# Performance work log

Hardware: AMD Instinct MI355X
Metric: run time of the kernel (lower is better)

Reference implementation:

```python
import jax, jax.numpy as jnp
import numpy as np

NEG_SLOPE = 0.01  # F.leaky_relu default in GATLayer.edge_attention
N_NODES = 50000
N_EDGES = 1600000
IN_DIM = 128
HEADS = 8
D_HEAD = 16  # out_dim / head_num = 128 / 8


def setup_inputs() -> dict:
    key = jax.random.key(0)
    ks = jax.random.split(key, 9)
    # glorot-ish scales for linear projections and attention vectors
    w_scale = (2.0 / (IN_DIM + D_HEAD)) ** 0.5
    a_scale = (2.0 / (2 * D_HEAD + 1)) ** 0.5
    return {
        "x": jax.random.normal(ks[0], (N_NODES, IN_DIM), dtype=jnp.float32),
        "src": jax.random.randint(ks[1], (N_EDGES,), 0, N_NODES, dtype=jnp.int32),
        "dst": jax.random.randint(ks[2], (N_EDGES,), 0, N_NODES, dtype=jnp.int32),
        "W1": jax.random.normal(ks[3], (HEADS, IN_DIM, D_HEAD), dtype=jnp.float32) * w_scale,
        "a1_src": jax.random.normal(ks[4], (HEADS, D_HEAD), dtype=jnp.float32) * a_scale,
        "a1_dst": jax.random.normal(ks[5], (HEADS, D_HEAD), dtype=jnp.float32) * a_scale,
        "W2": jax.random.normal(ks[6], (HEADS, IN_DIM, D_HEAD), dtype=jnp.float32) * w_scale,
        "a2_src": jax.random.normal(ks[7], (HEADS, D_HEAD), dtype=jnp.float32) * a_scale,
        "a2_dst": jax.random.normal(ks[8], (HEADS, D_HEAD), dtype=jnp.float32) * a_scale,
    }


def gat_multihead(h, src, dst, W, a_src, a_dst, num_nodes):
    """One MultiHeadLayer(GATLayer) with concat merge. h: [N, Din]."""
    z = jnp.einsum("nd,hdk->nhk", h, W)            # [N,H,Dh] per-head projection
    # attn_fc(cat(z_src, z_dst)) == a_src . z_src + a_dst . z_dst
    s_src = jnp.einsum("nhk,hk->nh", z, a_src)      # [N,H]
    s_dst = jnp.einsum("nhk,hk->nh", z, a_dst)      # [N,H]
    e = jax.nn.leaky_relu(s_src[src] + s_dst[dst], NEG_SLOPE)  # [E,H]
    # segment softmax over incoming edges of each dst node
    e_max = jax.ops.segment_max(e, dst, num_segments=num_nodes)          # [N,H]
    e_max = jnp.where(jnp.isfinite(e_max), e_max, 0.0)                   # empty segments
    w = jnp.exp(e - e_max[dst])                                          # [E,H]
    denom = jax.ops.segment_sum(w, dst, num_segments=num_nodes)          # [N,H]
    msg = w[:, :, None] * z[src]                                         # [E,H,Dh]
    num = jax.ops.segment_sum(msg, dst, num_segments=num_nodes)          # [N,H,Dh]
    out = num / jnp.where(denom == 0.0, 1.0, denom)[:, :, None]
    return out.reshape(num_nodes, -1)                                    # concat heads -> [N, H*Dh]


def reference(x, src, dst, W1, a1_src, a1_dst, W2, a2_src, a2_dst):
    n = x.shape[0]
    h = gat_multihead(x, src, dst, W1, a1_src, a1_dst, n)
    h = jax.nn.elu(h)
    h = gat_multihead(h, src, dst, W2, a2_src, a2_dst, n)
    return h
```

## Files before the change

### kernel.cpp

```cpp
#include <hip/hip_runtime.h>
#include <hip/hip_bf16.h>

#define N_NODES 50000
#define N_EDGES 1600000
#define NEG_SLOPE 0.01f
#define WPAD 136

#define NBKT 256
#define BKTW 196
#define NBLK1 200
#define CHUNK1 8000

typedef _Float16 v8h __attribute__((ext_vector_type(8)));
typedef _Float16 v2h __attribute__((ext_vector_type(2)));
typedef float v4f __attribute__((ext_vector_type(4)));

__global__ __launch_bounds__(256) void proj_mfma_kernel(
    const float* __restrict__ x,
    const float* __restrict__ W,
    _Float16* __restrict__ z)
{
    __shared__ _Float16 Wl[128 * WPAD];
    __shared__ _Float16 Zs[4][16][132];

    const int t = threadIdx.x;
    for (int i = t; i < 16384; i += 256) {
        const int h = i >> 11, k = (i >> 4) & 127, col = i & 15;
        Wl[(h * 16 + col) * WPAD + k] = (_Float16)W[i];
    }
    __syncthreads();

    const int wid = t >> 6;
    const int l   = t & 63;
    const int lc  = l & 15;
    const int kg  = l >> 4;

    const int nwaves = gridDim.x * 4;
    for (int tile = blockIdx.x * 4 + wid; tile < N_NODES / 16; tile += nwaves) {
        const int n0 = tile * 16;
        v4f acc[8];
#pragma unroll
        for (int ht = 0; ht < 8; ht++) acc[ht] = (v4f)0.f;

#pragma unroll
        for (int kb = 0; kb < 4; kb++) {
            const float4* xp = (const float4*)&x[(n0 + lc) * 128 + kb * 32 + kg * 8];
            const float4 xa = xp[0];
            const float4 xb = xp[1];
            v8h a;
            a[0] = (_Float16)xa.x; a[1] = (_Float16)xa.y;
            a[2] = (_Float16)xa.z; a[3] = (_Float16)xa.w;
            a[4] = (_Float16)xb.x; a[5] = (_Float16)xb.y;
            a[6] = (_Float16)xb.z; a[7] = (_Float16)xb.w;
#pragma unroll
            for (int ht = 0; ht < 8; ht++) {
                const v8h b = *(const v8h*)&Wl[(ht * 16 + lc) * WPAD + kb * 32 + kg * 8];
                acc[ht] = __builtin_amdgcn_mfma_f32_16x16x32_f16(a, b, acc[ht], 0, 0, 0);
            }
        }

#pragma unroll
        for (int ht = 0; ht < 8; ht++)
#pragma unroll
            for (int i = 0; i < 4; i++)
                Zs[wid][4 * kg + i][ht * 16 + lc] = (_Float16)acc[ht][i];

        const int r = l >> 2, q = l & 3;
        const _Float16* zr = &Zs[wid][r][q * 32];
        _Float16* zg = &z[(n0 + r) * 128 + q * 32];
#pragma unroll
        for (int c = 0; c < 4; c++)
            *(v8h*)(zg + c * 8) = *(const v8h*)(zr + c * 8);
    }
}

__global__ __launch_bounds__(256) void score_kernel(
    const _Float16* __restrict__ z,
    const float* __restrict__ a_src, const float* __restrict__ a_dst,
    float* __restrict__ s_src, float* __restrict__ s_dst)
{
    __shared__ float asl[128], adl[128];
    const int t = threadIdx.x;
    if (t < 128) { asl[t] = a_src[t]; adl[t] = a_dst[t]; }
    __syncthreads();

    const int idx = blockIdx.x * 256 + t;
    if (idx >= N_NODES * 8) return;
    const int n = idx >> 3, h = idx & 7;

    const v8h z0 = *(const v8h*)&z[n * 128 + h * 16];
    const v8h z1 = *(const v8h*)&z[n * 128 + h * 16 + 8];
    float ss = 0.f, sd = 0.f;
#pragma unroll
    for (int j = 0; j < 8; j++) {
        ss = fmaf((float)z0[j], asl[h * 16 + j], ss);
        sd = fmaf((float)z0[j], adl[h * 16 + j], sd);
    }
#pragma unroll
    for (int j = 0; j < 8; j++) {
        ss = fmaf((float)z1[j], asl[h * 16 + 8 + j], ss);
        sd = fmaf((float)z1[j], adl[h * 16 + 8 + j], sd);
    }
    s_src[idx] = ss;
    s_dst[idx] = sd;
}

__global__ __launch_bounds__(256) void hist_bucket_kernel(
    const int* __restrict__ dst, int* __restrict__ bh)
{
    __shared__ int lhist[NBKT];
    const int t = threadIdx.x, blk = blockIdx.x;
    lhist[t] = 0;
    __syncthreads();
    const int4* d4 = (const int4*)(dst + blk * CHUNK1);
    for (int i = t; i < CHUNK1 / 4; i += 256) {
        const int4 d = d4[i];
        atomicAdd(&lhist[(unsigned)d.x / BKTW], 1);
        atomicAdd(&lhist[(unsigned)d.y / BKTW], 1);
        atomicAdd(&lhist[(unsigned)d.z / BKTW], 1);
        atomicAdd(&lhist[(unsigned)d.w / BKTW], 1);
    }
    __syncthreads();
    bh[t * NBLK1 + blk] = lhist[t];
}

__global__ __launch_bounds__(256) void scan_buckets_kernel(
    int* __restrict__ bh, int* __restrict__ btotal)
{
    __shared__ int sb[256];
    const int t = threadIdx.x, b = blockIdx.x;
    const int v = (t < NBLK1) ? bh[b * NBLK1 + t] : 0;
    sb[t] = v;
    __syncthreads();
    int x = v;
    for (int off = 1; off < 256; off <<= 1) {
        const int add = (t >= off) ? sb[t - off] : 0;
        __syncthreads();
        x += add;
        sb[t] = x;
        __syncthreads();
    }
    if (t < NBLK1) bh[b * NBLK1 + t] = x - v;
    if (t == 255) btotal[b] = x;
}

__global__ __launch_bounds__(256) void scan_totals_kernel(
    const int* __restrict__ btotal, int* __restrict__ bstart)
{
    __shared__ int sb[256];
    const int t = threadIdx.x;
    const int v = btotal[t];
    sb[t] = v;
    __syncthreads();
    int x = v;
    for (int off = 1; off < 256; off <<= 1) {
        const int add = (t >= off) ? sb[t - off] : 0;
        __syncthreads();
        x += add;
        sb[t] = x;
        __syncthreads();
    }
    bstart[t] = x - v;
    if (t == 255) bstart[256] = x;
}

__global__ __launch_bounds__(256) void scatter_bucket_kernel(
    const int* __restrict__ src, const int* __restrict__ dst,
    const int* __restrict__ bh, const int* __restrict__ bstart,
    int* __restrict__ gbuf)
{
    __shared__ int lbase[NBKT];
    __shared__ int lcur[NBKT];
    const int t = threadIdx.x, blk = blockIdx.x;
    lbase[t] = bstart[t] + bh[t * NBLK1 + blk];
    lcur[t] = 0;
    __syncthreads();
    const int4* s4 = (const int4*)(src + blk * CHUNK1);
    const int4* d4 = (const int4*)(dst + blk * CHUNK1);
    for (int i = t; i < CHUNK1 / 4; i += 256) {
        const int4 d = d4[i];
        const int4 s = s4[i];
#pragma unroll
        for (int u = 0; u < 4; u++) {
            const int dd = (u == 0) ? d.x : (u == 1) ? d.y : (u == 2) ? d.z : d.w;
            const int ss = (u == 0) ? s.x : (u == 1) ? s.y : (u == 2) ? s.z : s.w;
            const unsigned b = (unsigned)dd / BKTW;
            const int ld = dd - (int)b * BKTW;
            const int r = atomicAdd(&lcur[b], 1);
            gbuf[lbase[b] + r] = (ld << 16) | ss;
        }
    }
}

__global__ __launch_bounds__(256) void sort_bucket_kernel(
    const int* __restrict__ gbuf, const int* __restrict__ bstart,
    int* __restrict__ perm, int* __restrict__ rowp)
{
    __shared__ int lhist[NBKT];
    __shared__ int lscan[NBKT];
    __shared__ int lcur[NBKT];
    const int t = threadIdx.x, b = blockIdx.x;
    const int base = bstart[b];
    const int cnt  = bstart[b + 1] - base;
    const int n0   = b * BKTW;

    lhist[t] = 0;
    lcur[t] = 0;
    __syncthreads();
    for (int i = t; i < cnt; i += 256)
        atomicAdd(&lhist[gbuf[base + i] >> 16], 1);
    __syncthreads();

    const int v = lhist[t];
    lscan[t] = v;
    __syncthreads();
    int x = v;
    for (int off = 1; off < 256; off <<= 1) {
        const int add = (t >= off) ? lscan[t - off] : 0;
        __syncthreads();
        x += add;
        lscan[t] = x;
        __syncthreads();
    }
    const int excl = x - v;
    __syncthreads();
    lscan[t] = excl;

    const int n = n0 + t;
    if (t < BKTW && n < N_NODES) rowp[n] = base + excl;
    if (b == NBKT - 1 && t == 0) rowp[N_NODES] = bstart[NBKT];
    __syncthreads();

    for (int i = t; i < cnt; i += 256) {
        const int e = gbuf[base + i];
        const int ld = e >> 16;
        const int r = atomicAdd(&lcur[ld], 1);
        perm[base + lscan[ld] + r] = (e & 0xFFFF) << 8;
    }
}

__global__ __launch_bounds__(256) void gather_kernel(
    const int* __restrict__ row_ptr, const int* __restrict__ perm,
    const char* __restrict__ zb,
    const char* __restrict__ ssb,
    const float* __restrict__ s_dst,
    float* __restrict__ out, const int apply_elu)
{
    const int wv = threadIdx.x >> 6;
    const int l  = threadIdx.x & 63;
    const int n  = blockIdx.x * 4 + wv;

    const int e8 = l >> 3;
    const int h8 = l & 7;
    const int h  = l >> 3;

    const int start = row_ptr[n];
    const int end   = row_ptr[n + 1];
    const float sd8 = s_dst[n * 8 + h8];

    float acc0 = 0.f, acc1 = 0.f, wsum = 0.f;

    for (int j0 = start; j0 < end; j0 += 8) {
        const int off = perm[j0 + e8];
        float s = *(const float*)(ssb + (off >> 3) + h8 * 4) + sd8;
        s = s > 0.f ? s : NEG_SLOPE * s;
        float w = __expf(s);
        w = (j0 + e8 < end) ? w : 0.f;

        int offk[8];
#pragma unroll
        for (int k = 0; k < 8; k++) offk[k] = __shfl(off, k * 8 + h);
        v2h zv[8];
#pragma unroll
        for (int k = 0; k < 8; k++)
            zv[k] = *(const v2h*)(zb + offk[k] + 4 * l);
#pragma unroll
        for (int k = 0; k < 8; k++) {
            const float wk = __shfl(w, k * 8 + h);
            wsum += wk;
            acc0 = fmaf(wk, (float)zv[k][0], acc0);
            acc1 = fmaf(wk, (float)zv[k][1], acc1);
        }
    }

    const float inv = (end > start) ? 1.f / wsum : 0.f;
    float o0 = acc0 * inv;
    float o1 = acc1 * inv;
    if (apply_elu) {
        o0 = o0 > 0.f ? o0 : expm1f(o0);
        o1 = o1 > 0.f ? o1 : expm1f(o1);
    }
    *(float2*)&out[n * 128 + 2 * l] = make_float2(o0, o1);
}

extern "C" void kernel_launch(void* const* d_in, const int* in_sizes, int n_in,
                              void* d_out, int out_size, void* d_ws, size_t ws_size,
                              hipStream_t stream) {
    const float* x    = (const float*)d_in[0];
    const int*   src  = (const int*)d_in[1];
    const int*   dst  = (const int*)d_in[2];
    const float* W1   = (const float*)d_in[3];
    const float* a1s  = (const float*)d_in[4];
    const float* a1d  = (const float*)d_in[5];
    const float* W2   = (const float*)d_in[6];
    const float* a2s  = (const float*)d_in[7];
    const float* a2d  = (const float*)d_in[8];
    float* out = (float*)d_out;

    char* p = (char*)d_ws;
    _Float16* z  = (_Float16*)p;  p += (size_t)N_NODES * 128 * 2;
    float* ssrc  = (float*)p;     p += (size_t)N_NODES * 8 * 4;
    float* sdst  = (float*)p;     p += (size_t)N_NODES * 8 * 4;
    int*   rowp  = (int*)p;       p += ((size_t)N_NODES + 4) * 4;
    int*   bh    = (int*)p;       p += (size_t)NBKT * NBLK1 * 4;
    int*   btot  = (int*)p;       p += (size_t)NBKT * 4;
    int*   bstart= (int*)p;       p += ((size_t)NBKT + 4) * 4;
    int*   gbuf  = (int*)p;       p += (size_t)N_EDGES * 4;
    int*   perm  = (int*)p;       p += ((size_t)N_EDGES + 8) * 4;

    const int PROJ_GRID   = 391;
    const int SCORE_GRID  = (N_NODES * 8 + 255) / 256;
    const int NODE4_GRID  = N_NODES / 4;

    hipMemsetAsync(perm + N_EDGES, 0, 8 * 4, stream);
    hist_bucket_kernel<<<NBLK1, 256, 0, stream>>>(dst, bh);
    scan_buckets_kernel<<<NBKT, 256, 0, stream>>>(bh, btot);
    scan_totals_kernel<<<1, 256, 0, stream>>>(btot, bstart);
    scatter_bucket_kernel<<<NBLK1, 256, 0, stream>>>(src, dst, bh, bstart, gbuf);
    sort_bucket_kernel<<<NBKT, 256, 0, stream>>>(gbuf, bstart, perm, rowp);

    proj_mfma_kernel<<<PROJ_GRID, 256, 0, stream>>>(x, W1, z);
    score_kernel<<<SCORE_GRID, 256, 0, stream>>>(z, a1s, a1d, ssrc, sdst);
    gather_kernel<<<NODE4_GRID, 256, 0, stream>>>(rowp, perm, (const char*)z,
                                                  (const char*)ssrc, sdst, out, 1);

    proj_mfma_kernel<<<PROJ_GRID, 256, 0, stream>>>(out, W2, z);
    score_kernel<<<SCORE_GRID, 256, 0, stream>>>(z, a2s, a2d, ssrc, sdst);
    gather_kernel<<<NODE4_GRID, 256, 0, stream>>>(rowp, perm, (const char*)z,
                                                  (const char*)ssrc, sdst, out, 0);
}
```

Baseline: 214.0 us.

## Fuse attention scores into projection and co-launch first projection with histogram

Attention scores are now computed inside the MFMA projection kernel from the tile already held in shared memory, which removes the separate score kernel and its re-read of z. The first projection is also merged with the bucket histogram into one launch with disjoint block ranges, so the two independent stages run concurrently. Together these cut two or three kernel launches. The cost is extra shared memory and register use in the projection blocks, and heterogeneous blocks sharing one launch.

```diff
diff --git a/kernel.cpp b/kernel.cpp
--- a/kernel.cpp
+++ b/kernel.cpp
@@ -11,23 +11,28 @@
 #define NBLK1 200
 #define CHUNK1 8000
 
+#define PROJ_GRID 391
+
 typedef _Float16 v8h __attribute__((ext_vector_type(8)));
 typedef _Float16 v2h __attribute__((ext_vector_type(2)));
 typedef float v4f __attribute__((ext_vector_type(4)));
 
-__global__ __launch_bounds__(256) void proj_mfma_kernel(
-    const float* __restrict__ x,
-    const float* __restrict__ W,
-    _Float16* __restrict__ z)
+__device__ __forceinline__ void proj_body(
+    const float* __restrict__ x, const float* __restrict__ W,
+    const float* __restrict__ a_src, const float* __restrict__ a_dst,
+    _Float16* __restrict__ z, float* __restrict__ s_src,
+    float* __restrict__ s_dst, const int blk, const int nblocks)
 {
     __shared__ _Float16 Wl[128 * WPAD];
     __shared__ _Float16 Zs[4][16][132];
+    __shared__ float asl[128], adl[128];
 
     const int t = threadIdx.x;
     for (int i = t; i < 16384; i += 256) {
         const int h = i >> 11, k = (i >> 4) & 127, col = i & 15;
         Wl[(h * 16 + col) * WPAD + k] = (_Float16)W[i];
     }
+    if (t < 128) { asl[t] = a_src[t]; adl[t] = a_dst[t]; }
     __syncthreads();
 
     const int wid = t >> 6;
@@ -35,8 +40,8 @@
     const int lc  = l & 15;
     const int kg  = l >> 4;
 
-    const int nwaves = gridDim.x * 4;
-    for (int tile = blockIdx.x * 4 + wid; tile < N_NODES / 16; tile += nwaves) {
+    const int nwaves = nblocks * 4;
+    for (int tile = blk * 4 + wid; tile < N_NODES / 16; tile += nwaves) {
         const int n0 = tile * 16;
         v4f acc[8];
 #pragma unroll
@@ -67,49 +72,44 @@
 
         const int r = l >> 2, q = l & 3;
         const _Float16* zr = &Zs[wid][r][q * 32];
+        v8h vv[4];
+#pragma unroll
+        for (int c = 0; c < 4; c++) vv[c] = *(const v8h*)(zr + c * 8);
+
+        float s0s = 0.f, s1s = 0.f, s0d = 0.f, s1d = 0.f;
+#pragma unroll
+        for (int c = 0; c < 2; c++)
+#pragma unroll
+            for (int j = 0; j < 8; j++) {
+                const float zf = (float)vv[c][j];
+                const int ch = q * 32 + c * 8 + j;
+                s0s = fmaf(zf, asl[ch], s0s);
+                s0d = fmaf(zf, adl[ch], s0d);
+            }
+#pragma unroll
+        for (int c = 2; c < 4; c++)
+#pragma unroll
+            for (int j = 0; j < 8; j++) {
+                const float zf = (float)vv[c][j];
+                const int ch = q * 32 + c * 8 + j;
+                s1s = fmaf(zf, asl[ch], s1s);
+                s1d = fmaf(zf, adl[ch], s1d);
+            }
+
         _Float16* zg = &z[(n0 + r) * 128 + q * 32];
 #pragma unroll
         for (int c = 0; c < 4; c++)
-            *(v8h*)(zg + c * 8) = *(const v8h*)(zr + c * 8);
-    }
-}
-
-__global__ __launch_bounds__(256) void score_kernel(
-    const _Float16* __restrict__ z,
-    const float* __restrict__ a_src, const float* __restrict__ a_dst,
-    float* __restrict__ s_src, float* __restrict__ s_dst)
-{
-    __shared__ float asl[128], adl[128];
+            *(v8h*)(zg + c * 8) = vv[c];
+        *(float2*)&s_src[(n0 + r) * 8 + 2 * q] = make_float2(s0s, s1s);
+        *(float2*)&s_dst[(n0 + r) * 8 + 2 * q] = make_float2(s0d, s1d);
+    }
+}
+
+__device__ __forceinline__ void hist_body(
+    const int* __restrict__ dst, int* __restrict__ bh, const int blk)
+{
+    __shared__ int lhist[NBKT];
     const int t = threadIdx.x;
-    if (t < 128) { asl[t] = a_src[t]; adl[t] = a_dst[t]; }
-    __syncthreads();
-
-    const int idx = blockIdx.x * 256 + t;
-    if (idx >= N_NODES * 8) return;
-    const int n = idx >> 3, h = idx & 7;
-
-    const v8h z0 = *(const v8h*)&z[n * 128 + h * 16];
-    const v8h z1 = *(const v8h*)&z[n * 128 + h * 16 + 8];
-    float ss = 0.f, sd = 0.f;
-#pragma unroll
-    for (int j = 0; j < 8; j++) {
-        ss = fmaf((float)z0[j], asl[h * 16 + j], ss);
-        sd = fmaf((float)z0[j], adl[h * 16 + j], sd);
-    }
-#pragma unroll
-    for (int j = 0; j < 8; j++) {
-        ss = fmaf((float)z1[j], asl[h * 16 + 8 + j], ss);
-        sd = fmaf((float)z1[j], adl[h * 16 + 8 + j], sd);
-    }
-    s_src[idx] = ss;
-    s_dst[idx] = sd;
-}
-
-__global__ __launch_bounds__(256) void hist_bucket_kernel(
-    const int* __restrict__ dst, int* __restrict__ bh)
-{
-    __shared__ int lhist[NBKT];
-    const int t = threadIdx.x, blk = blockIdx.x;
     lhist[t] = 0;
     __syncthreads();
     const int4* d4 = (const int4*)(dst + blk * CHUNK1);
@@ -122,6 +122,28 @@
     }
     __syncthreads();
     bh[t * NBLK1 + blk] = lhist[t];
+}
+
+__global__ __launch_bounds__(256) void proj_hist_kernel(
+    const float* __restrict__ x, const float* __restrict__ W,
+    const float* __restrict__ a_src, const float* __restrict__ a_dst,
+    _Float16* __restrict__ z, float* __restrict__ s_src,
+    float* __restrict__ s_dst,
+    const int* __restrict__ dst, int* __restrict__ bh)
+{
+    if (blockIdx.x < PROJ_GRID)
+        proj_body(x, W, a_src, a_dst, z, s_src, s_dst, blockIdx.x, PROJ_GRID);
+    else
+        hist_body(dst, bh, blockIdx.x - PROJ_GRID);
+}
+
+__global__ __launch_bounds__(256) void proj_kernel(
+    const float* __restrict__ x, const float* __restrict__ W,
+    const float* __restrict__ a_src, const float* __restrict__ a_dst,
+    _Float16* __restrict__ z, float* __restrict__ s_src,
+    float* __restrict__ s_dst)
+{
+    proj_body(x, W, a_src, a_dst, z, s_src, s_dst, blockIdx.x, PROJ_GRID);
 }
 
 __global__ __launch_bounds__(256) void scan_buckets_kernel(
@@ -318,24 +340,20 @@
     int*   gbuf  = (int*)p;       p += (size_t)N_EDGES * 4;
     int*   perm  = (int*)p;       p += ((size_t)N_EDGES + 8) * 4;
 
-    const int PROJ_GRID   = 391;
-    const int SCORE_GRID  = (N_NODES * 8 + 255) / 256;
-    const int NODE4_GRID  = N_NODES / 4;
+    const int NODE4_GRID = N_NODES / 4;
 
     hipMemsetAsync(perm + N_EDGES, 0, 8 * 4, stream);
-    hist_bucket_kernel<<<NBLK1, 256, 0, stream>>>(dst, bh);
+
+    proj_hist_kernel<<<PROJ_GRID + NBLK1, 256, 0, stream>>>(
+        x, W1, a1s, a1d, z, ssrc, sdst, dst, bh);
     scan_buckets_kernel<<<NBKT, 256, 0, stream>>>(bh, btot);
     scan_totals_kernel<<<1, 256, 0, stream>>>(btot, bstart);
     scatter_bucket_kernel<<<NBLK1, 256, 0, stream>>>(src, dst, bh, bstart, gbuf);
     sort_bucket_kernel<<<NBKT, 256, 0, stream>>>(gbuf, bstart, perm, rowp);
-
-    proj_mfma_kernel<<<PROJ_GRID, 256, 0, stream>>>(x, W1, z);
-    score_kernel<<<SCORE_GRID, 256, 0, stream>>>(z, a1s, a1d, ssrc, sdst);
     gather_kernel<<<NODE4_GRID, 256, 0, stream>>>(rowp, perm, (const char*)z,
                                                   (const char*)ssrc, sdst, out, 1);
 
-    proj_mfma_kernel<<<PROJ_GRID, 256, 0, stream>>>(out, W2, z);
-    score_kernel<<<SCORE_GRID, 256, 0, stream>>>(z, a2s, a2d, ssrc, sdst);
+    proj_kernel<<<PROJ_GRID, 256, 0, stream>>>(out, W2, a2s, a2d, z, ssrc, sdst);
     gather_kernel<<<NODE4_GRID, 256, 0, stream>>>(rowp, perm, (const char*)z,
                                                   (const char*)ssrc, sdst, out, 0);
 }
```

After: 219.4 us. 2.5% more time.
